# Kernel tuning notes

Hardware: AMD Instinct MI355X
Metric: run time of the kernel (lower is better)

## Reference

```python
import jax, jax.numpy as jnp
import numpy as np

N_LAYERS = 3


def setup_inputs() -> dict:
    key = jax.random.key(0)
    k1, k2, k3, k4 = jax.random.split(key, 4)
    user_emb = jax.random.normal(k1, (29858, 64), dtype=jnp.float32)
    item_emb = jax.random.normal(k2, (40981, 64), dtype=jnp.float32)
    v = jax.random.normal(k3, (70839, 512), dtype=jnp.float32)
    filters = jax.random.normal(k4, (N_LAYERS, 512), dtype=jnp.float32)
    return {"user_emb": user_emb, "item_emb": item_emb, "v": v, "filters": filters}


def reference(user_emb, item_emb, v, filters):
    # ego: [N, D], v: [N, F], filters: [L, F]
    n_users = user_emb.shape[0]
    ego = jnp.concatenate([user_emb, item_emb], axis=0)
    acc = ego  # running sum for the mean over (layers + 1) embeddings
    for k in range(filters.shape[0]):
        # V @ diag(f) @ V^T @ ego  ==  V @ (f[:, None] * (V^T @ ego))
        proj = v.T @ ego                      # [F, D]
        ego = v @ (filters[k][:, None] * proj)  # [N, D]
        acc = acc + ego
    all_emb = acc / (filters.shape[0] + 1)
    return all_emb[:n_users], all_emb[n_users:]
```

## Files before the change

kernel.cpp:

```cpp
#include <hip/hip_runtime.h>
#include <hip/hip_bf16.h>


#define N_USERS 29858
#define N_TOTAL 70839
#define DQ 64
#define FD 512
#define NPAD 71168
#define NC 35
#define CHUNK 2048

typedef __attribute__((ext_vector_type(8))) short short8;
typedef __attribute__((ext_vector_type(4))) short short4v;
typedef __attribute__((ext_vector_type(4))) float f32x4;
typedef unsigned int u32;
typedef unsigned short u16;

static __device__ __forceinline__ u32 f32u(float x){union{float f;u32 u;}a;a.f=x;return a.u;}
static __device__ __forceinline__ float uf32(u32 u){union{u32 u;float f;}a;a.u=u;return a.f;}
static __device__ __forceinline__ u32 pack_h(u32 x0, u32 x1){
  return __builtin_amdgcn_perm(x1, x0, 0x07060302u);
}
static __device__ __forceinline__ void split_pair(u32 x0, u32 x1, u32& hp, u32& lp) {
  hp = pack_h(x0, x1);
  u32 l0 = f32u(uf32(x0) - uf32(x0 & 0xFFFF0000u));
  u32 l1 = f32u(uf32(x1) - uf32(x1 & 0xFFFF0000u));
  lp = pack_h(l0, l1);
}
union U8x { u32 u[4]; short8 s; };

static __device__ __forceinline__ u16 bf16_rne(float x) {
  u32 u = f32u(x);
  return (u16)((u + 0x7FFFu + ((u >> 16) & 1u)) >> 16);
}
static __device__ __forceinline__ void split2(float x, u16& h, u16& l) {
  h = bf16_rne(x);
  l = bf16_rne(x - uf32(((u32)h) << 16));
}

static __device__ __forceinline__ void load_lds16(const float* g, float* l) {
  __builtin_amdgcn_global_load_lds(
      (const __attribute__((address_space(1))) u32*)(g),
      (__attribute__((address_space(3))) u32*)(l), 16, 0, 0);
}

__global__ __launch_bounds__(256) void init_kernel(
    const float* __restrict__ u, const float* __restrict__ it,
    float* __restrict__ out, u16* __restrict__ egoT_h, u16* __restrict__ egoT_l) {
  const int n0 = blockIdx.x * 64;
  const int t = threadIdx.x;
  const int nq = t & 15, dq = t >> 4;
  f32x4 rows[4];
#pragma unroll
  for (int r = 0; r < 4; ++r) {
    int n = n0 + nq * 4 + r;
    f32x4 val = {0.f, 0.f, 0.f, 0.f};
    if (n < N_TOTAL) {
      const float* src = (n < N_USERS) ? (u + (size_t)n * DQ)
                                       : (it + (size_t)(n - N_USERS) * DQ);
      val = *(const f32x4*)(src + dq * 4);
      *(f32x4*)(out + (size_t)n * DQ + dq * 4) = val;
    }
    rows[r] = val;
  }
#pragma unroll
  for (int i = 0; i < 4; ++i) {
    int d = dq * 4 + i;
    short4v hv, lv;
#pragma unroll
    for (int r = 0; r < 4; ++r) {
      u16 h, l;
      split2(rows[r][i], h, l);
      hv[r] = (short)h; lv[r] = (short)l;
    }
    *(short4v*)(egoT_h + (size_t)d * NPAD + n0 + nq * 4) = hv;
    *(short4v*)(egoT_l + (size_t)d * NPAD + n0 + nq * 4) = lv;
  }
}

__global__ __launch_bounds__(256, 2) void gram_kernel(
    const float* __restrict__ v, const u16* __restrict__ egoT_h,
    const u16* __restrict__ egoT_l, float* __restrict__ parts) {
  __shared__ short8 HAh[1024];
  __shared__ short8 HAl[1024];
  __shared__ short8 HBh[256];
  __shared__ short8 HBl[256];

  const int job = blockIdx.x;
  const int n0c = blockIdx.y * CHUNK;
  const int nend = min(n0c + CHUNK, NPAD);
  const bool isC0 = (job >= 12);
  const int itile = isC0 ? (job - 12) : (job < 8 ? 0 : 1);
  const int fA = itile * 256;
  const int jcol = isC0 ? 0 : (job < 8 ? job : job - 4);
  const int colbase = jcol * 64;
  const bool reuseB = !isC0 && (colbase >= fA) && (colbase + 64 <= fA + 256);
  const bool stageB = !isC0 && !reuseB;
  const int cb0q = reuseB ? ((colbase - fA) >> 6) : 0;

  const int t = threadIdx.x;
  const int lane = t & 63, wv = t >> 6;
  const int m16 = lane & 15, quad = lane >> 4;
  const int fl = lane, nq = wv;

  f32x4 acc[4][4];
#pragma unroll
  for (int a = 0; a < 4; ++a)
#pragma unroll
    for (int b = 0; b < 4; ++b) acc[a][b] = (f32x4){0.f, 0.f, 0.f, 0.f};

  u32 xA[4][8];
  u32 xB[8];
  short8 xBh, xBl;

  auto issue = [&](int n0) {
#pragma unroll
    for (int seg = 0; seg < 4; ++seg)
#pragma unroll
      for (int r = 0; r < 8; ++r) {
        int n = n0 + nq * 8 + r;
        xA[seg][r] = (n < N_TOTAL) ? f32u(v[(size_t)n * FD + fA + seg * 64 + fl]) : 0u;
      }
    if (stageB) {
#pragma unroll
      for (int r = 0; r < 8; ++r) {
        int n = n0 + nq * 8 + r;
        xB[r] = (n < N_TOTAL) ? f32u(v[(size_t)n * FD + colbase + fl]) : 0u;
      }
    }
    if (isC0) {
      xBh = *(const short8*)(egoT_h + (size_t)fl * NPAD + n0 + nq * 8);
      xBl = *(const short8*)(egoT_l + (size_t)fl * NPAD + n0 + nq * 8);
    }
  };

  issue(n0c);

  for (int n0 = n0c; n0 < nend; n0 += 32) {
    asm volatile("s_barrier" ::: "memory");

    const int uw = (fl & 15) + ((fl >> 4) & 3) * 64 + nq * 16;
#pragma unroll
    for (int seg = 0; seg < 4; ++seg) {
      U8x H, L;
#pragma unroll
      for (int p = 0; p < 4; ++p)
        split_pair(xA[seg][2 * p], xA[seg][2 * p + 1], H.u[p], L.u[p]);
      HAh[uw + seg * 256] = H.s;
      HAl[uw + seg * 256] = L.s;
    }
    if (stageB) {
      U8x H, L;
#pragma unroll
      for (int p = 0; p < 4; ++p)
        split_pair(xB[2 * p], xB[2 * p + 1], H.u[p], L.u[p]);
      HBh[uw] = H.s;
      HBl[uw] = L.s;
    } else if (isC0) {
      HBh[uw] = xBh;
      HBl[uw] = xBl;
    }

    if (n0 + 32 < nend) issue(n0 + 32);

    asm volatile("s_waitcnt lgkmcnt(0)" ::: "memory");
    asm volatile("s_barrier" ::: "memory");

    short8 ah[4], al[4];
#pragma unroll
    for (int mt = 0; mt < 4; ++mt) {
      int u = m16 + mt * 64 + wv * 256 + quad * 16;
      ah[mt] = HAh[u];
      al[mt] = HAl[u];
    }
#pragma unroll
    for (int ct = 0; ct < 4; ++ct) {
      short8 bh, bl;
      if (reuseB) {
        int u = m16 + ct * 64 + cb0q * 256 + quad * 16;
        bh = HAh[u]; bl = HAl[u];
      } else {
        int u = m16 + ct * 64 + quad * 16;
        bh = HBh[u]; bl = HBl[u];
      }
#pragma unroll
      for (int mt = 0; mt < 4; ++mt) {
        acc[mt][ct] = __builtin_amdgcn_mfma_f32_16x16x32_bf16(ah[mt], bh, acc[mt][ct], 0, 0, 0);
        acc[mt][ct] = __builtin_amdgcn_mfma_f32_16x16x32_bf16(ah[mt], bl, acc[mt][ct], 0, 0, 0);
        acc[mt][ct] = __builtin_amdgcn_mfma_f32_16x16x32_bf16(al[mt], bh, acc[mt][ct], 0, 0, 0);
      }
    }
  }

  float* pb = parts + (size_t)blockIdx.y * (512 * 576);
  const int cb = isC0 ? 512 : colbase;
#pragma unroll
  for (int mt = 0; mt < 4; ++mt) {
    int row = fA + wv * 64 + mt * 16 + quad * 4;
#pragma unroll
    for (int ct = 0; ct < 4; ++ct) {
      int col = cb + ct * 16 + m16;
#pragma unroll
      for (int reg = 0; reg < 4; ++reg)
        pb[(size_t)(row + reg) * 576 + col] = acc[mt][ct][reg];
    }
  }
}

__global__ __launch_bounds__(256) void finalize_kernel(
    const float* __restrict__ parts, float* __restrict__ G, float* __restrict__ c0) {
  int idx = blockIdx.x * 256 + threadIdx.x;
  int r = idx / 576, c = idx % 576;
  float s = 0.f;
  if (c >= 512) {
    for (int p = 0; p < NC; ++p) s += parts[(size_t)p * (512 * 576) + r * 576 + c];
    c0[r * 64 + (c - 512)] = s;
  } else {
    bool direct = (c >> 6) >= 4 * (r >> 8);
    int rr = direct ? r : c, cc = direct ? c : r;
    for (int p = 0; p < NC; ++p) s += parts[(size_t)p * (512 * 576) + rr * 576 + cc];
    G[r * 512 + c] = s;
  }
}

__global__ __launch_bounds__(256) void apply_g_kernel(
    const float* __restrict__ G, const float* __restrict__ filt,
    const float* __restrict__ cin, float* __restrict__ cout) {
  __shared__ float red[4][64];
  const int t = threadIdx.x;
  const int i = blockIdx.x;
  const int sub = t >> 6, d = t & 63;
  float s = 0.f;
#pragma unroll 8
  for (int j = sub * 128; j < (sub + 1) * 128; ++j)
    s += G[i * 512 + j] * (filt[j] * cin[j * 64 + d]);
  red[sub][d] = s;
  __syncthreads();
  if (sub == 0)
    cout[i * 64 + d] = red[0][d] + red[1][d] + red[2][d] + red[3][d];
}

__global__ __launch_bounds__(256) void prep_wt_kernel(
    const float* __restrict__ filters, const float* __restrict__ c0,
    const float* __restrict__ c1, const float* __restrict__ c2,
    u16* __restrict__ wt_h, u16* __restrict__ wt_l) {
  int idx = blockIdx.x * 256 + threadIdx.x;
  int d = idx >> 9, f = idx & 511;
  float w = filters[f] * c0[f * 64 + d] + filters[512 + f] * c1[f * 64 + d] +
            filters[1024 + f] * c2[f * 64 + d];
  u32 xu = f32u(w);
  u32 h = xu & 0xFFFF0000u;
  u32 lu = f32u(w - uf32(h));
  wt_h[d * FD + f] = (u16)(xu >> 16);
  wt_l[d * FD + f] = (u16)(lu >> 16);
}

__global__ __launch_bounds__(256) void expand_kernel(
    const float* __restrict__ v, const u16* __restrict__ wt_h,
    const u16* __restrict__ wt_l, float* __restrict__ out) {
  __shared__ float raw[2][128 * 64];
  const int t = threadIdx.x;
  const int lane = t & 63, wv = t >> 6;
  const int m16 = lane & 15, quad = lane >> 4;
  const int nb = blockIdx.x * 128;

  f32x4 acc[2][4];
#pragma unroll
  for (int a = 0; a < 2; ++a)
#pragma unroll
    for (int b = 0; b < 4; ++b) acc[a][b] = (f32x4){0.f, 0.f, 0.f, 0.f};

  auto stage = [&](int buf, int fs) {
#pragma unroll
    for (int g = 0; g < 8; ++g) {
      int rl = g * 4 + (lane >> 4);
      int sw = rl & 7;
      int grow = min(nb + wv * 32 + rl, N_TOTAL - 1);
      const float* gp = v + (size_t)grow * FD + fs + (((lane & 15) ^ sw) << 2);
      load_lds16(gp, &raw[buf][(wv * 32 + g * 4) * 64]);
    }
  };

  stage(0, 0);
  for (int it = 0; it < 8; ++it) {
    const int buf = it & 1, fs = it * 64;
    short8 pbh[2][4], pbl[2][4];
#pragma unroll
    for (int k = 0; k < 2; ++k)
#pragma unroll
      for (int ct = 0; ct < 4; ++ct) {
        const size_t off = (size_t)(ct * 16 + m16) * FD + fs + k * 32 + quad * 8;
        pbh[k][ct] = *(const short8*)(wt_h + off);
        pbl[k][ct] = *(const short8*)(wt_l + off);
      }
    asm volatile("" ::: "memory");
    if (it + 1 < 8) {
      stage(buf ^ 1, fs + 64);
      asm volatile("s_waitcnt vmcnt(24)" ::: "memory");
    } else {
      asm volatile("s_waitcnt vmcnt(16)" ::: "memory");
    }
#pragma unroll
    for (int k0i = 0; k0i < 2; ++k0i) {
      short8 ah[2], al[2];
#pragma unroll
      for (int mt = 0; mt < 2; ++mt) {
        const float* rb = &raw[buf][(wv * 32 + mt * 16 + m16) * 64];
        const int sw = m16 & 7;
        const int j0 = k0i * 8 + quad * 2;
        f32x4 xa = *(const f32x4*)(rb + ((j0 ^ sw) << 2));
        f32x4 xb = *(const f32x4*)(rb + (((j0 + 1) ^ sw) << 2));
        U8x H, L;
        split_pair(f32u(xa[0]), f32u(xa[1]), H.u[0], L.u[0]);
        split_pair(f32u(xa[2]), f32u(xa[3]), H.u[1], L.u[1]);
        split_pair(f32u(xb[0]), f32u(xb[1]), H.u[2], L.u[2]);
        split_pair(f32u(xb[2]), f32u(xb[3]), H.u[3], L.u[3]);
        ah[mt] = H.s; al[mt] = L.s;
      }
#pragma unroll
      for (int ct = 0; ct < 4; ++ct) {
#pragma unroll
        for (int mt = 0; mt < 2; ++mt) {
          acc[mt][ct] = __builtin_amdgcn_mfma_f32_16x16x32_bf16(ah[mt], pbh[k0i][ct], acc[mt][ct], 0, 0, 0);
          acc[mt][ct] = __builtin_amdgcn_mfma_f32_16x16x32_bf16(ah[mt], pbl[k0i][ct], acc[mt][ct], 0, 0, 0);
          acc[mt][ct] = __builtin_amdgcn_mfma_f32_16x16x32_bf16(al[mt], pbh[k0i][ct], acc[mt][ct], 0, 0, 0);
        }
      }
    }
  }

#pragma unroll
  for (int mt = 0; mt < 2; ++mt) {
    int nrow = nb + wv * 32 + mt * 16 + quad * 4;
#pragma unroll
    for (int ct = 0; ct < 4; ++ct) {
      int d = ct * 16 + m16;
#pragma unroll
      for (int reg = 0; reg < 4; ++reg) {
        int n = nrow + reg;
        if (n < N_TOTAL) {
          float* op = out + (size_t)n * DQ + d;
          *op = (*op + acc[mt][ct][reg]) * 0.25f;
        }
      }
    }
  }
}

extern "C" void kernel_launch(void* const* d_in, const int* in_sizes, int n_in,
                              void* d_out, int out_size, void* d_ws, size_t ws_size,
                              hipStream_t stream) {
  const float* user_emb = (const float*)d_in[0];
  const float* item_emb = (const float*)d_in[1];
  const float* v        = (const float*)d_in[2];
  const float* filters  = (const float*)d_in[3];
  float* out = (float*)d_out;

  u16* egoT_h = (u16*)d_ws;
  u16* egoT_l = egoT_h + (size_t)DQ * NPAD;
  float* parts = (float*)(egoT_l + (size_t)DQ * NPAD);
  float* G     = parts + (size_t)NC * 512 * 576;
  float* c0    = G + 512 * 512;
  float* c1    = c0 + 512 * 64;
  float* c2    = c1 + 512 * 64;
  u16* wt_h    = (u16*)(c2 + 512 * 64);
  u16* wt_l    = wt_h + (size_t)DQ * FD;

  init_kernel<<<NPAD / 64, 256, 0, stream>>>(user_emb, item_emb, out, egoT_h, egoT_l);
  gram_kernel<<<dim3(14, NC), 256, 0, stream>>>(v, egoT_h, egoT_l, parts);
  finalize_kernel<<<(512 * 576) / 256, 256, 0, stream>>>(parts, G, c0);
  apply_g_kernel<<<512, 256, 0, stream>>>(G, filters, c0, c1);
  apply_g_kernel<<<512, 256, 0, stream>>>(G, filters + 512, c1, c2);
  prep_wt_kernel<<<128, 256, 0, stream>>>(filters, c0, c1, c2, wt_h, wt_l);
  expand_kernel<<<NPAD / 128, 256, 0, stream>>>(v, wt_h, wt_l, out);
}
```

Measured before the change: 467.4 us.

## Block the split ego layout per 32-row tile and size gram chunks from workspace

The init kernel now transposes ego through an LDS tile and writes high/low bf16 halves into a blocked layout, one contiguous 8 KB block per 32 rows. The gram kernel then reads each C0 tile with one coalesced load per thread instead of strided per-feature rows. The number of gram partial chunks is now derived from workspace size, capped at 70, so the grid can have up to twice as many blocks for better occupancy. The cost is that finalize has more partial sums to reduce, and correctness now depends on the available workspace.

```diff
diff --git a/kernel.cpp b/kernel.cpp
--- a/kernel.cpp
+++ b/kernel.cpp
@@ -7,8 +7,6 @@
 #define DQ 64
 #define FD 512
 #define NPAD 71168
-#define NC 35
-#define CHUNK 2048
 
 typedef __attribute__((ext_vector_type(8))) short short8;
 typedef __attribute__((ext_vector_type(4))) short short4v;
@@ -44,51 +42,67 @@
       (__attribute__((address_space(3))) u32*)(l), 16, 0, 0);
 }
 
+
 __global__ __launch_bounds__(256) void init_kernel(
     const float* __restrict__ u, const float* __restrict__ it,
-    float* __restrict__ out, u16* __restrict__ egoT_h, u16* __restrict__ egoT_l) {
+    float* __restrict__ out, u16* __restrict__ egoTb) {
+  __shared__ float tile[64][65];
   const int n0 = blockIdx.x * 64;
   const int t = threadIdx.x;
-  const int nq = t & 15, dq = t >> 4;
-  f32x4 rows[4];
-#pragma unroll
-  for (int r = 0; r < 4; ++r) {
-    int n = n0 + nq * 4 + r;
-    f32x4 val = {0.f, 0.f, 0.f, 0.f};
+  const int r = t >> 2, cbase = (t & 3) * 16;
+  {
+    int n = n0 + r;
     if (n < N_TOTAL) {
       const float* src = (n < N_USERS) ? (u + (size_t)n * DQ)
                                        : (it + (size_t)(n - N_USERS) * DQ);
-      val = *(const f32x4*)(src + dq * 4);
-      *(f32x4*)(out + (size_t)n * DQ + dq * 4) = val;
-    }
-    rows[r] = val;
-  }
-#pragma unroll
-  for (int i = 0; i < 4; ++i) {
-    int d = dq * 4 + i;
-    short4v hv, lv;
-#pragma unroll
-    for (int r = 0; r < 4; ++r) {
-      u16 h, l;
-      split2(rows[r][i], h, l);
-      hv[r] = (short)h; lv[r] = (short)l;
-    }
-    *(short4v*)(egoT_h + (size_t)d * NPAD + n0 + nq * 4) = hv;
-    *(short4v*)(egoT_l + (size_t)d * NPAD + n0 + nq * 4) = lv;
+#pragma unroll
+      for (int q = 0; q < 4; ++q) {
+        f32x4 val = *(const f32x4*)(src + cbase + q * 4);
+        *(f32x4*)(out + (size_t)n * DQ + cbase + q * 4) = val;
+        tile[r][cbase + q * 4 + 0] = val[0];
+        tile[r][cbase + q * 4 + 1] = val[1];
+        tile[r][cbase + q * 4 + 2] = val[2];
+        tile[r][cbase + q * 4 + 3] = val[3];
+      }
+    } else {
+#pragma unroll
+      for (int q = 0; q < 4; ++q)
+#pragma unroll
+        for (int e = 0; e < 4; ++e) tile[r][cbase + q * 4 + e] = 0.f;
+    }
+  }
+  __syncthreads();
+  const int s = t;
+  const int d = (s & 15) | ((s >> 6) << 4);
+  const int nb = (s >> 4) & 3;
+#pragma unroll
+  for (int sl = 0; sl < 2; ++sl) {
+    U8x H, L;
+#pragma unroll
+    for (int j = 0; j < 4; ++j) {
+      u16 h0, l0, h1, l1;
+      split2(tile[sl * 32 + nb * 8 + 2 * j][d], h0, l0);
+      split2(tile[sl * 32 + nb * 8 + 2 * j + 1][d], h1, l1);
+      H.u[j] = (u32)h0 | ((u32)h1 << 16);
+      L.u[j] = (u32)l0 | ((u32)l1 << 16);
+    }
+    size_t base = (size_t)(blockIdx.x * 2 + sl) * 4096;
+    *(short8*)(egoTb + base + (size_t)s * 8) = H.s;
+    *(short8*)(egoTb + base + 2048 + (size_t)s * 8) = L.s;
   }
 }
 
 __global__ __launch_bounds__(256, 2) void gram_kernel(
-    const float* __restrict__ v, const u16* __restrict__ egoT_h,
-    const u16* __restrict__ egoT_l, float* __restrict__ parts) {
+    const float* __restrict__ v, const u16* __restrict__ egoTb,
+    float* __restrict__ parts, int chunk) {
   __shared__ short8 HAh[1024];
   __shared__ short8 HAl[1024];
   __shared__ short8 HBh[256];
   __shared__ short8 HBl[256];
 
   const int job = blockIdx.x;
-  const int n0c = blockIdx.y * CHUNK;
-  const int nend = min(n0c + CHUNK, NPAD);
+  const int n0c = blockIdx.y * chunk;
+  const int nend = min(n0c + chunk, NPAD);
   const bool isC0 = (job >= 12);
   const int itile = isC0 ? (job - 12) : (job < 8 ? 0 : 1);
   const int fA = itile * 256;
@@ -114,6 +128,10 @@
   short8 xBh, xBl;
 
   auto issue = [&](int n0) {
+    if (isC0) {
+      xBh = *(const short8*)(egoTb + (size_t)(n0 >> 5) * 4096 + (size_t)t * 8);
+      xBl = *(const short8*)(egoTb + (size_t)(n0 >> 5) * 4096 + 2048 + (size_t)t * 8);
+    }
 #pragma unroll
     for (int seg = 0; seg < 4; ++seg)
 #pragma unroll
@@ -127,10 +145,6 @@
         int n = n0 + nq * 8 + r;
         xB[r] = (n < N_TOTAL) ? f32u(v[(size_t)n * FD + colbase + fl]) : 0u;
       }
-    }
-    if (isC0) {
-      xBh = *(const short8*)(egoT_h + (size_t)fl * NPAD + n0 + nq * 8);
-      xBl = *(const short8*)(egoT_l + (size_t)fl * NPAD + n0 + nq * 8);
     }
   };
 
@@ -157,8 +171,8 @@
       HBh[uw] = H.s;
       HBl[uw] = L.s;
     } else if (isC0) {
-      HBh[uw] = xBh;
-      HBl[uw] = xBl;
+      HBh[t] = xBh;
+      HBl[t] = xBl;
     }
 
     if (n0 + 32 < nend) issue(n0 + 32);
@@ -208,17 +222,18 @@
 }
 
 __global__ __launch_bounds__(256) void finalize_kernel(
-    const float* __restrict__ parts, float* __restrict__ G, float* __restrict__ c0) {
+    const float* __restrict__ parts, int nc,
+    float* __restrict__ G, float* __restrict__ c0) {
   int idx = blockIdx.x * 256 + threadIdx.x;
   int r = idx / 576, c = idx % 576;
   float s = 0.f;
   if (c >= 512) {
-    for (int p = 0; p < NC; ++p) s += parts[(size_t)p * (512 * 576) + r * 576 + c];
+    for (int p = 0; p < nc; ++p) s += parts[(size_t)p * (512 * 576) + r * 576 + c];
     c0[r * 64 + (c - 512)] = s;
   } else {
     bool direct = (c >> 6) >= 4 * (r >> 8);
     int rr = direct ? r : c, cc = direct ? c : r;
-    for (int p = 0; p < NC; ++p) s += parts[(size_t)p * (512 * 576) + rr * 576 + cc];
+    for (int p = 0; p < nc; ++p) s += parts[(size_t)p * (512 * 576) + rr * 576 + cc];
     G[r * 512 + c] = s;
   }
 }
@@ -282,8 +297,8 @@
   };
 
   stage(0, 0);
-  for (int it = 0; it < 8; ++it) {
-    const int buf = it & 1, fs = it * 64;
+  for (int it8 = 0; it8 < 8; ++it8) {
+    const int buf = it8 & 1, fs = it8 * 64;
     short8 pbh[2][4], pbl[2][4];
 #pragma unroll
     for (int k = 0; k < 2; ++k)
@@ -294,7 +309,7 @@
         pbl[k][ct] = *(const short8*)(wt_l + off);
       }
     asm volatile("" ::: "memory");
-    if (it + 1 < 8) {
+    if (it8 + 1 < 8) {
       stage(buf ^ 1, fs + 64);
       asm volatile("s_waitcnt vmcnt(24)" ::: "memory");
     } else {
@@ -356,19 +371,28 @@
   const float* filters  = (const float*)d_in[3];
   float* out = (float*)d_out;
 
-  u16* egoT_h = (u16*)d_ws;
-  u16* egoT_l = egoT_h + (size_t)DQ * NPAD;
-  float* parts = (float*)(egoT_l + (size_t)DQ * NPAD);
-  float* G     = parts + (size_t)NC * 512 * 576;
+  const size_t EGOTB_BYTES = (size_t)(NPAD / 32) * 8192;
+  const size_t SMALL_BYTES = (512 * 512 + 3 * 512 * 64) * 4 + 2 * DQ * FD * 2;
+  size_t avail = ws_size > EGOTB_BYTES + SMALL_BYTES
+                     ? ws_size - EGOTB_BYTES - SMALL_BYTES : 0;
+  int nc = (int)(avail / ((size_t)512 * 576 * 4));
+  if (nc > 70) nc = 70;
+  if (nc < 1) nc = 1;
+  int chunk = ((NPAD + nc - 1) / nc + 31) & ~31;
+  int ncA = (NPAD + chunk - 1) / chunk;
+
+  u16* egoTb  = (u16*)d_ws;
+  float* parts = (float*)((char*)d_ws + EGOTB_BYTES);
+  float* G     = parts + (size_t)ncA * 512 * 576;
   float* c0    = G + 512 * 512;
   float* c1    = c0 + 512 * 64;
   float* c2    = c1 + 512 * 64;
   u16* wt_h    = (u16*)(c2 + 512 * 64);
   u16* wt_l    = wt_h + (size_t)DQ * FD;
 
-  init_kernel<<<NPAD / 64, 256, 0, stream>>>(user_emb, item_emb, out, egoT_h, egoT_l);
-  gram_kernel<<<dim3(14, NC), 256, 0, stream>>>(v, egoT_h, egoT_l, parts);
-  finalize_kernel<<<(512 * 576) / 256, 256, 0, stream>>>(parts, G, c0);
+  init_kernel<<<NPAD / 64, 256, 0, stream>>>(user_emb, item_emb, out, egoTb);
+  gram_kernel<<<dim3(14, ncA), 256, 0, stream>>>(v, egoTb, parts, chunk);
+  finalize_kernel<<<(512 * 576) / 256, 256, 0, stream>>>(parts, ncA, G, c0);
   apply_g_kernel<<<512, 256, 0, stream>>>(G, filters, c0, c1);
   apply_g_kernel<<<512, 256, 0, stream>>>(G, filters + 512, c1, c2);
   prep_wt_kernel<<<128, 256, 0, stream>>>(filters, c0, c1, c2, wt_h, wt_l);
```

New measurement: 476.6 us. No clear change (+2.0%).
